# Performance work log

Hardware: AMD Instinct MI355X
Metric: run time of the kernel (lower is better)

Reference implementation:

```python
import jax, jax.numpy as jnp
import numpy as np

HIDDEN = 1024
N_EXPERTS = 8
CAP_FACTOR = 1.1
LN_EPS = 1e-5


def setup_inputs() -> dict:
    key = jax.random.key(0)
    ks = jax.random.split(key, 8)
    d, E, dff = HIDDEN, N_EXPERTS, 4 * HIDDEN
    x = jax.random.normal(ks[0], (4, 2048, d), dtype=jnp.float32)
    gate_w = jax.random.normal(ks[1], (d, E), dtype=jnp.float32) / np.sqrt(d)
    ln_g = jnp.ones((E, d), dtype=jnp.float32)
    ln_b = jnp.zeros((E, d), dtype=jnp.float32)
    w1 = jax.random.normal(ks[2], (E, d, dff), dtype=jnp.float32) / np.sqrt(d)
    b1 = jnp.zeros((E, dff), dtype=jnp.float32)
    w2 = jax.random.normal(ks[3], (E, dff, d), dtype=jnp.float32) / np.sqrt(dff)
    b2 = jnp.zeros((E, d), dtype=jnp.float32)
    return {"x": x, "gate_w": gate_w, "ln_g": ln_g, "ln_b": ln_b,
            "w1": w1, "b1": b1, "w2": w2, "b2": b2}


def reference(x, gate_w, ln_g, ln_b, w1, b1, w2, b2):
    B, S, d = x.shape
    E = gate_w.shape[1]
    N = B * S
    cap = int(N / E * CAP_FACTOR)  # expert capacity

    xt = x.reshape(N, d)
    # Router: top-1 expert per token (max-subtract before softmax is a no-op)
    logits = xt @ gate_w                               # [N, E]
    probs = jax.nn.softmax(logits, axis=-1)
    eidx = jnp.argmax(probs, axis=-1)                  # [N] int

    onehot = jax.nn.one_hot(eidx, E, dtype=jnp.int32)  # [N, E]
    counts = onehot.sum(axis=0).astype(jnp.float32)    # pre-drop counts [E]

    # Deterministic capacity: keep first `cap` tokens per expert, drop rest.
    # (torch code drops randomly via multinomial; structure is identical.)
    pos = jnp.cumsum(onehot, axis=0) - 1               # [N, E]
    pos_tok = jnp.take_along_axis(pos, eidx[:, None], axis=1)[:, 0]  # [N]
    keep = (pos_tok < cap).astype(x.dtype)             # [N]
    pos_c = jnp.minimum(pos_tok, cap - 1)              # clamp; dropped tokens write zeros

    # Dispatch into per-expert buffers [E, cap, d]
    buf = jnp.zeros((E, cap, d), dtype=x.dtype).at[eidx, pos_c].add(xt * keep[:, None])

    # Per-expert FFN: LayerNorm -> Linear -> GELU -> Linear
    mu = buf.mean(axis=-1, keepdims=True)
    var = jnp.mean((buf - mu) ** 2, axis=-1, keepdims=True)
    nb = (buf - mu) * jax.lax.rsqrt(var + LN_EPS)
    nb = nb * ln_g[:, None, :] + ln_b[:, None, :]
    h = jax.nn.gelu(jnp.einsum('ecd,edf->ecf', nb, w1) + b1[:, None, :], approximate=False)
    y = jnp.einsum('ecf,efd->ecd', h, w2) + b2[:, None, :]  # [E, cap, d]

    # Combine: dropped tokens get zeros (matches torch output init)
    out_tok = y[eidx, pos_c] * keep[:, None]           # [N, d]
    output = out_tok.reshape(B, S, d)

    # Load-balancing loss: 1 - cosine(counts, uniform) * 0.01
    tokens_per_expert = N / E
    uniform = jnp.full((E,), tokens_per_expert, dtype=jnp.float32)
    cos = jnp.dot(counts, uniform) / (jnp.linalg.norm(counts) * jnp.linalg.norm(uniform) + 1e-8)
    loss = 1.0 - cos * 0.01
    return output, loss
```

## Files before the change

kernel.cpp:

```cpp
#include <hip/hip_runtime.h>
#include <cstdint>
#include <cstddef>

#define NTOK 8192
#define D    1024
#define DFF  4096
#define NEXP 8
#define CAP  1126
#define MROWS 1280

typedef float f32x4 __attribute__((ext_vector_type(4)));
typedef __bf16 bf16x8 __attribute__((ext_vector_type(8)));

__device__ inline unsigned short f2bf(float f) {
    unsigned u = __float_as_uint(f);
    u += 0x7fffu + ((u >> 16) & 1u);
    return (unsigned short)(u >> 16);
}

__device__ inline float gelu(float x) {
    float z  = 0.70710678118654752f * x;
    float az = fabsf(z);
    float t  = 1.0f / fmaf(0.3275911f, az, 1.0f);
    float p  = t * fmaf(t, fmaf(t, fmaf(t, fmaf(t, 1.061405429f, -1.453152027f),
                                        1.421413741f), -0.284496736f), 0.254829592f);
    float ee = __expf(-az * az);
    float er = fmaf(-p, ee, 1.0f);
    er = __builtin_copysignf(er, z);
    return 0.5f * x * (1.0f + er);
}

__device__ inline void gload16(const void* g, void* l) {
    __builtin_amdgcn_global_load_lds(
        (const __attribute__((address_space(1))) unsigned int*)g,
        (__attribute__((address_space(3))) unsigned int*)l,
        16, 0, 0);
}

__device__ void transpose_tile_dev(const float* __restrict__ W, unsigned short* __restrict__ WT,
                                   int K, int N, int tb, char* smem)
{
    int tiles_k = K >> 7, tiles_n = N >> 7;
    int per_e = tiles_k * tiles_n;
    int e = tb / per_e, rem = tb % per_e;
    int kb = rem % tiles_k, nb = rem / tiles_k;
    const float* We = W + (size_t)e * K * N + (size_t)(kb * 128) * N + nb * 128;
    unsigned short* Oe = WT + (size_t)e * K * N + (size_t)(nb * 128) * K + kb * 128;
    float* lds = (float*)smem;
    int t = threadIdx.x;
    #pragma unroll
    for (int p = 0; p < 2; ++p) {
        __syncthreads();
        #pragma unroll
        for (int j = 0; j < 8; ++j) {
            int idx = j * 256 + t;
            int r = idx >> 5, c4 = idx & 31;
            const float4 v = *(const float4*)(We + (size_t)(p * 64 + r) * N + c4 * 4);
            *(float4*)(lds + r * 128 + c4 * 4) = v;
        }
        __syncthreads();
        int c = t >> 1, half = t & 1;
        const float* col = lds + (half * 32) * 128 + c;
        unsigned short* orow = Oe + (size_t)c * K + p * 64 + half * 32;
        #pragma unroll
        for (int q = 0; q < 4; ++q) {
            uint4 o;
            o.x = f2bf(col[(q*8+0)*128]) | ((unsigned)f2bf(col[(q*8+1)*128]) << 16);
            o.y = f2bf(col[(q*8+2)*128]) | ((unsigned)f2bf(col[(q*8+3)*128]) << 16);
            o.z = f2bf(col[(q*8+4)*128]) | ((unsigned)f2bf(col[(q*8+5)*128]) << 16);
            o.w = f2bf(col[(q*8+6)*128]) | ((unsigned)f2bf(col[(q*8+7)*128]) << 16);
            *(uint4*)(orow + q * 8) = o;
        }
    }
}

__global__ __launch_bounds__(256) void transpose_kernel(
    const float* __restrict__ W, unsigned short* __restrict__ WT, int K, int N)
{
    __shared__ __align__(16) char smem[32768];
    transpose_tile_dev(W, WT, K, N, blockIdx.x, smem);
}

__global__ __launch_bounds__(256) void router_kernel(
    const float* __restrict__ x, const float* __restrict__ gw, int* __restrict__ eidx)
{
    int tok  = blockIdx.x * 4 + (threadIdx.x >> 6);
    int lane = threadIdx.x & 63;
    const float* xr = x + (size_t)tok * D;
    float a[8] = {0.f,0.f,0.f,0.f,0.f,0.f,0.f,0.f};
    #pragma unroll
    for (int it = 0; it < D / 64; ++it) {
        int d = lane + it * 64;
        float xv = xr[d];
        const float4 g0 = *(const float4*)(gw + (size_t)d * 8);
        const float4 g1 = *(const float4*)(gw + (size_t)d * 8 + 4);
        a[0] += xv * g0.x; a[1] += xv * g0.y; a[2] += xv * g0.z; a[3] += xv * g0.w;
        a[4] += xv * g1.x; a[5] += xv * g1.y; a[6] += xv * g1.z; a[7] += xv * g1.w;
    }
    #pragma unroll
    for (int off = 32; off > 0; off >>= 1)
        #pragma unroll
        for (int e = 0; e < 8; ++e) a[e] += __shfl_xor(a[e], off, 64);
    if (lane == 0) {
        int bi = 0; float bv = a[0];
        #pragma unroll
        for (int e = 1; e < 8; ++e) if (a[e] > bv) { bv = a[e]; bi = e; }
        eidx[tok] = bi;
    }
}

__global__ __launch_bounds__(1024) void scan_kernel(
    const int* __restrict__ eidx, int* __restrict__ slot_map,
    int* __restrict__ kept_cnt, float* __restrict__ loss_out,
    int* __restrict__ droplist, int* __restrict__ dropcnt)
{
    __shared__ int sc[8][1024];
    __shared__ int dcnt;
    int t = threadIdx.x;
    if (t == 0) dcnt = 0;
    int le[8];
    int c[8] = {0,0,0,0,0,0,0,0};
    #pragma unroll
    for (int i = 0; i < 8; ++i) { le[i] = eidx[t * 8 + i]; c[le[i]]++; }
    int v[8];
    #pragma unroll
    for (int e = 0; e < 8; ++e) { v[e] = c[e]; sc[e][t] = v[e]; }
    __syncthreads();
    for (int s = 1; s < 1024; s <<= 1) {
        int add[8] = {0,0,0,0,0,0,0,0};
        if (t >= s) {
            #pragma unroll
            for (int e = 0; e < 8; ++e) add[e] = sc[e][t - s];
        }
        __syncthreads();
        #pragma unroll
        for (int e = 0; e < 8; ++e) { v[e] += add[e]; sc[e][t] = v[e]; }
        __syncthreads();
    }
    int base[8];
    #pragma unroll
    for (int e = 0; e < 8; ++e) base[e] = v[e] - c[e];
    #pragma unroll
    for (int i = 0; i < 8; ++i) {
        int e = le[i]; int pos = base[e]++;
        if (pos < CAP) slot_map[e * CAP + pos] = t * 8 + i;
        else { int s = atomicAdd(&dcnt, 1); droplist[s] = t * 8 + i; }
    }
    __syncthreads();
    if (t == 0) *dropcnt = dcnt;
    if (t == 1023) {
        float dotv = 0.f, ss = 0.f;
        #pragma unroll
        for (int e = 0; e < 8; ++e) {
            float cf = (float)v[e];
            kept_cnt[e] = v[e] < CAP ? v[e] : CAP;
            dotv += cf * 1024.0f;
            ss   += cf * cf;
        }
        float denom = sqrtf(ss) * (1024.0f * sqrtf(8.0f)) + 1e-8f;
        loss_out[0] = 1.0f - 0.01f * (dotv / denom);
    }
}

__global__ __launch_bounds__(256) void zero_dropped(
    const int* __restrict__ droplist, const int* __restrict__ dropcnt,
    float4* __restrict__ out)
{
    int n = (*dropcnt) * 256;
    for (int idx = blockIdx.x * 256 + threadIdx.x; idx < n; idx += gridDim.x * 256)
        out[(size_t)droplist[idx >> 8] * 256 + (idx & 255)] = make_float4(0.f,0.f,0.f,0.f);
}

__global__ __launch_bounds__(256) void dispatch_ln(
    const float* __restrict__ x, const float* __restrict__ lng, const float* __restrict__ lnb,
    const int* __restrict__ slot_map, const int* __restrict__ kept_cnt,
    unsigned short* __restrict__ xbuf)
{
    int p = blockIdx.x, e = blockIdx.y, tid = threadIdx.x;
    ushort4* dst = (ushort4*)(xbuf + ((size_t)e * MROWS + p) * D) + tid;
    if (p >= kept_cnt[e]) { *dst = make_ushort4(0, 0, 0, 0); return; }
    int tok = slot_map[e * CAP + p];
    const float4 xv = *((const float4*)(x + (size_t)tok * D) + tid);
    float s  = xv.x + xv.y + xv.z + xv.w;
    float ss = xv.x * xv.x + xv.y * xv.y + xv.z * xv.z + xv.w * xv.w;
    #pragma unroll
    for (int off = 32; off > 0; off >>= 1) {
        s  += __shfl_xor(s,  off, 64);
        ss += __shfl_xor(ss, off, 64);
    }
    __shared__ float red[8];
    int lane = tid & 63, wv = tid >> 6;
    if (lane == 0) { red[wv] = s; red[4 + wv] = ss; }
    __syncthreads();
    s  = red[0] + red[1] + red[2] + red[3];
    ss = red[4] + red[5] + red[6] + red[7];
    float mu = s * (1.0f / D);
    float rs = rsqrtf(ss * (1.0f / D) - mu * mu + 1e-5f);
    const float4 gv = *((const float4*)(lng + (size_t)e * D) + tid);
    const float4 bv = *((const float4*)(lnb + (size_t)e * D) + tid);
    ushort4 o;
    o.x = f2bf((xv.x - mu) * rs * gv.x + bv.x);
    o.y = f2bf((xv.y - mu) * rs * gv.y + bv.y);
    o.z = f2bf((xv.z - mu) * rs * gv.z + bv.z);
    o.w = f2bf((xv.w - mu) * rs * gv.w + bv.w);
    *dst = o;
}

template<int K, int N, int MODE>
__global__ __launch_bounds__(512, 2) void gemm_kernel(
    const unsigned short* __restrict__ A,
    const unsigned short* __restrict__ BT,
    const float* __restrict__ bias,
    unsigned short* __restrict__ Hout,
    float* __restrict__ Yout,
    const int* __restrict__ slot_map,
    const int* __restrict__ kept_cnt)
{
    constexpr int MB = MROWS / 256;
    constexpr int NB = N / 256;
    constexpr int GB = NEXP * MB * NB;
    constexpr int T  = K / 64;
    __shared__ __align__(16) char smem[131072];

    const int obid = blockIdx.x;
    const int q8 = GB >> 3, r8 = GB & 7;
    const int xcd = obid & 7, ii = obid >> 3;
    const int swz = (xcd < r8 ? xcd * (q8 + 1) : r8 * (q8 + 1) + (xcd - r8) * q8) + ii;
    const int mb = swz % MB;
    const int t2 = swz / MB;
    const int nb = t2 % NB;
    const int e  = t2 / NB;

    const int tid  = threadIdx.x;
    const int lane = tid & 63;
    const int l15  = lane & 15, lg = lane >> 4;
    const int wave = tid >> 6;
    const int wr = wave >> 2, wc = wave & 3;
    const unsigned short* Ae = A + ((size_t)e * MROWS + (size_t)mb * 256) * K;
    const unsigned short* Be = BT + ((size_t)e * N + (size_t)nb * 256) * K;
    f32x4 acc[8][4] = {};

    auto stageAB = [&](int buf, int kk) {
        char* sA = smem + buf * 65536;
        char* sB = sA + 32768;
        #pragma unroll
        for (int q = 0; q < 4; ++q) {
            int cid = q * 512 + tid;
            int row = cid >> 3, pp = cid & 7;
            int cc  = pp ^ ((row >> 1) & 7);
            gload16(Ae + (size_t)row * K + kk * 64 + cc * 8, sA + cid * 16);
            gload16(Be + (size_t)row * K + kk * 64 + cc * 8, sB + cid * 16);
        }
    };
    auto quad_load = [&](const char* sA, const char* sB, int mh, int nh,
                         bf16x8 (&af)[2][4], bf16x8 (&bfv)[2][2]) {
        #pragma unroll
        for (int i = 0; i < 4; ++i) {
            int ra = wr * 128 + mh * 64 + i * 16 + l15;
            #pragma unroll
            for (int ks = 0; ks < 2; ++ks)
                af[ks][i] = *(const bf16x8*)(sA + ra * 128 +
                             (((ks * 4 + lg) ^ ((ra >> 1) & 7)) << 4));
        }
        #pragma unroll
        for (int jn = 0; jn < 2; ++jn) {
            int rb = wc * 64 + nh * 32 + jn * 16 + l15;
            #pragma unroll
            for (int ks = 0; ks < 2; ++ks)
                bfv[ks][jn] = *(const bf16x8*)(sB + rb * 128 +
                             (((ks * 4 + lg) ^ ((rb >> 1) & 7)) << 4));
        }
    };
    auto quad_mfma = [&](int mh, int nh, bf16x8 (&af)[2][4], bf16x8 (&bfv)[2][2]) {
        __builtin_amdgcn_s_setprio(1);
        #pragma unroll
        for (int ks = 0; ks < 2; ++ks)
            #pragma unroll
            for (int i = 0; i < 4; ++i)
                #pragma unroll
                for (int jn = 0; jn < 2; ++jn)
                    acc[mh * 4 + i][nh * 2 + jn] = __builtin_amdgcn_mfma_f32_16x16x32_bf16(
                        bfv[ks][jn], af[ks][i], acc[mh * 4 + i][nh * 2 + jn], 0, 0, 0);
        __builtin_amdgcn_s_setprio(0);
    };

    stageAB(0, 0);
    stageAB(1, 1);
    asm volatile("s_waitcnt vmcnt(8)" ::: "memory");
    __builtin_amdgcn_s_barrier();

    for (int t = 0; t < T; ++t) {
        const char* sA = smem + (t & 1) * 65536;
        const char* sB = sA + 32768;
        bf16x8 af[2][4]; bf16x8 bfv[2][2];
        quad_load(sA, sB, 0, 0, af, bfv);  quad_mfma(0, 0, af, bfv);
        __builtin_amdgcn_sched_barrier(0);
        quad_load(sA, sB, 0, 1, af, bfv);  quad_mfma(0, 1, af, bfv);
        __builtin_amdgcn_sched_barrier(0);
        quad_load(sA, sB, 1, 0, af, bfv);  quad_mfma(1, 0, af, bfv);
        __builtin_amdgcn_sched_barrier(0);
        quad_load(sA, sB, 1, 1, af, bfv);
        asm volatile("s_waitcnt lgkmcnt(0)" ::: "memory");
        __builtin_amdgcn_sched_barrier(0);
        __builtin_amdgcn_s_barrier();
        if (t + 2 < T) stageAB(t & 1, t + 2);
        __builtin_amdgcn_sched_barrier(0);
        quad_mfma(1, 1, af, bfv);
        if (t < T - 1) {
            if (t + 2 < T) asm volatile("s_waitcnt vmcnt(8)" ::: "memory");
            else           asm volatile("s_waitcnt vmcnt(0)" ::: "memory");
            __builtin_amdgcn_s_barrier();
        }
    }

    const int kept = (MODE == 1) ? kept_cnt[e] : 0;
    #pragma unroll
    for (int mi = 0; mi < 8; ++mi) {
        const int row = mb * 256 + wr * 128 + mi * 16 + l15;
        int tok = 0; bool live = true;
        if (MODE == 1) {
            live = row < kept;
            tok = live ? slot_map[e * CAP + row] : 0;
        }
        #pragma unroll
        for (int ni = 0; ni < 4; ++ni) {
            const int colb = nb * 256 + wc * 64 + ni * 16 + 4 * lg;
            const float4 bv = *(const float4*)(bias + (size_t)e * N + colb);
            if (MODE == 0) {
                ushort4 o;
                o.x = f2bf(gelu(acc[mi][ni][0] + bv.x));
                o.y = f2bf(gelu(acc[mi][ni][1] + bv.y));
                o.z = f2bf(gelu(acc[mi][ni][2] + bv.z));
                o.w = f2bf(gelu(acc[mi][ni][3] + bv.w));
                *(ushort4*)(Hout + ((size_t)e * MROWS + row) * N + colb) = o;
            } else if (live) {
                float4 o = make_float4(acc[mi][ni][0] + bv.x, acc[mi][ni][1] + bv.y,
                                       acc[mi][ni][2] + bv.z, acc[mi][ni][3] + bv.w);
                *(float4*)(Yout + (size_t)tok * D + colb) = o;
            }
        }
    }
}

extern "C" void kernel_launch(void* const* d_in, const int* in_sizes, int n_in,
                              void* d_out, int out_size, void* d_ws, size_t ws_size,
                              hipStream_t stream)
{
    const float* x   = (const float*)d_in[0];
    const float* gw  = (const float*)d_in[1];
    const float* lng = (const float*)d_in[2];
    const float* lnb = (const float*)d_in[3];
    const float* w1  = (const float*)d_in[4];
    const float* b1  = (const float*)d_in[5];
    const float* w2  = (const float*)d_in[6];
    const float* b2  = (const float*)d_in[7];
    float* out = (float*)d_out;
    char* ws = (char*)d_ws;

    unsigned short* wT   = (unsigned short*)ws;
    unsigned short* xbuf = (unsigned short*)(ws + 67108864);
    unsigned short* hbuf = (unsigned short*)(ws + 88080384);
    int* eidx     = (int*)(ws + 171966464);
    int* slot_map = eidx + NTOK;
    int* kept     = slot_map + NEXP * CAP;
    int* dropcnt  = kept + NEXP;
    int* droplist = dropcnt + 8;

    constexpr int GB1 = NEXP * (MROWS / 256) * (DFF / 256);
    constexpr int GB2 = NEXP * (MROWS / 256) * (D / 256);
    constexpr int TB1 = NEXP * (D / 128) * (DFF / 128);
    constexpr int TB2 = NEXP * (DFF / 128) * (D / 128);

    router_kernel<<<NTOK / 4, 256, 0, stream>>>(x, gw, eidx);
    scan_kernel<<<1, 1024, 0, stream>>>(eidx, slot_map, kept,
                                        out + (size_t)NTOK * D, droplist, dropcnt);
    zero_dropped<<<64, 256, 0, stream>>>(droplist, dropcnt, (float4*)out);
    dispatch_ln<<<dim3(MROWS, NEXP), 256, 0, stream>>>(x, lng, lnb, slot_map, kept, xbuf);

    transpose_kernel<<<TB1, 256, 0, stream>>>(w1, wT, D, DFF);
    gemm_kernel<D, DFF, 0><<<GB1, 512, 0, stream>>>(
        xbuf, wT, b1, hbuf, nullptr, slot_map, kept);

    transpose_kernel<<<TB2, 256, 0, stream>>>(w2, wT, DFF, D);
    gemm_kernel<DFF, D, 1><<<GB2, 512, 0, stream>>>(
        hbuf, wT, b2, nullptr, out, slot_map, kept);
}
```

Baseline: 380.4 us.

## Switch expert GEMM to 32x32x16 MFMA tiles with two-phase LDS loads

Replaces the 16x16x32 bf16 MFMA with the 32x32x16 variant, so each wave computes its 128x64 tile as 4x2 blocks of 32x32 with 16-float accumulators. The four quarter-steps per K tile become two halves that each load all A/B fragments, then issue 16 MFMAs. Larger MFMA tiles cut LDS fragment reads and instruction count per FLOP. The cost is less overlap between LDS loads and MFMAs, and a changed epilogue mapping of accumulator lanes to output rows and columns.

```diff
diff --git a/kernel.cpp b/kernel.cpp
--- a/kernel.cpp
+++ b/kernel.cpp
@@ -9,7 +9,8 @@
 #define CAP  1126
 #define MROWS 1280
 
-typedef float f32x4 __attribute__((ext_vector_type(4)));
+typedef float f32x4  __attribute__((ext_vector_type(4)));
+typedef float f32x16 __attribute__((ext_vector_type(16)));
 typedef __bf16 bf16x8 __attribute__((ext_vector_type(8)));
 
 __device__ inline unsigned short f2bf(float f) {
@@ -233,12 +234,12 @@
 
     const int tid  = threadIdx.x;
     const int lane = tid & 63;
-    const int l15  = lane & 15, lg = lane >> 4;
+    const int l31  = lane & 31, hi = lane >> 5;
     const int wave = tid >> 6;
     const int wr = wave >> 2, wc = wave & 3;
     const unsigned short* Ae = A + ((size_t)e * MROWS + (size_t)mb * 256) * K;
     const unsigned short* Be = BT + ((size_t)e * N + (size_t)nb * 256) * K;
-    f32x4 acc[8][4] = {};
+    f32x16 acc[4][2] = {};
 
     auto stageAB = [&](int buf, int kk) {
         char* sA = smem + buf * 65536;
@@ -252,36 +253,15 @@
             gload16(Be + (size_t)row * K + kk * 64 + cc * 8, sB + cid * 16);
         }
     };
-    auto quad_load = [&](const char* sA, const char* sB, int mh, int nh,
-                         bf16x8 (&af)[2][4], bf16x8 (&bfv)[2][2]) {
-        #pragma unroll
-        for (int i = 0; i < 4; ++i) {
-            int ra = wr * 128 + mh * 64 + i * 16 + l15;
-            #pragma unroll
-            for (int ks = 0; ks < 2; ++ks)
-                af[ks][i] = *(const bf16x8*)(sA + ra * 128 +
-                             (((ks * 4 + lg) ^ ((ra >> 1) & 7)) << 4));
-        }
-        #pragma unroll
-        for (int jn = 0; jn < 2; ++jn) {
-            int rb = wc * 64 + nh * 32 + jn * 16 + l15;
-            #pragma unroll
-            for (int ks = 0; ks < 2; ++ks)
-                bfv[ks][jn] = *(const bf16x8*)(sB + rb * 128 +
-                             (((ks * 4 + lg) ^ ((rb >> 1) & 7)) << 4));
-        }
+    auto ldA = [&](const char* sA, int mblk, int ks) -> bf16x8 {
+        int row = wr * 128 + mblk * 32 + l31;
+        int c0  = 2 * ks + hi;
+        return *(const bf16x8*)(sA + row * 128 + ((c0 ^ ((row >> 1) & 7)) << 4));
     };
-    auto quad_mfma = [&](int mh, int nh, bf16x8 (&af)[2][4], bf16x8 (&bfv)[2][2]) {
-        __builtin_amdgcn_s_setprio(1);
-        #pragma unroll
-        for (int ks = 0; ks < 2; ++ks)
-            #pragma unroll
-            for (int i = 0; i < 4; ++i)
-                #pragma unroll
-                for (int jn = 0; jn < 2; ++jn)
-                    acc[mh * 4 + i][nh * 2 + jn] = __builtin_amdgcn_mfma_f32_16x16x32_bf16(
-                        bfv[ks][jn], af[ks][i], acc[mh * 4 + i][nh * 2 + jn], 0, 0, 0);
-        __builtin_amdgcn_s_setprio(0);
+    auto ldB = [&](const char* sB, int nblk, int ks) -> bf16x8 {
+        int row = wc * 64 + nblk * 32 + l31;
+        int c0  = 2 * ks + hi;
+        return *(const bf16x8*)(sB + row * 128 + ((c0 ^ ((row >> 1) & 7)) << 4));
     };
 
     stageAB(0, 0);
@@ -292,20 +272,43 @@
     for (int t = 0; t < T; ++t) {
         const char* sA = smem + (t & 1) * 65536;
         const char* sB = sA + 32768;
-        bf16x8 af[2][4]; bf16x8 bfv[2][2];
-        quad_load(sA, sB, 0, 0, af, bfv);  quad_mfma(0, 0, af, bfv);
+        bf16x8 af[4][2], bfv[2][2];
+        #pragma unroll
+        for (int m = 0; m < 4; ++m) { af[m][0] = ldA(sA, m, 0); af[m][1] = ldA(sA, m, 1); }
+        #pragma unroll
+        for (int n = 0; n < 2; ++n) { bfv[n][0] = ldB(sB, n, 0); bfv[n][1] = ldB(sB, n, 1); }
+        asm volatile("s_waitcnt lgkmcnt(0)" ::: "memory");
         __builtin_amdgcn_sched_barrier(0);
-        quad_load(sA, sB, 0, 1, af, bfv);  quad_mfma(0, 1, af, bfv);
+        __builtin_amdgcn_s_setprio(1);
+        #pragma unroll
+        for (int ks = 0; ks < 2; ++ks)
+            #pragma unroll
+            for (int m = 0; m < 4; ++m)
+                #pragma unroll
+                for (int n = 0; n < 2; ++n)
+                    acc[m][n] = __builtin_amdgcn_mfma_f32_32x32x16_bf16(
+                        bfv[n][ks], af[m][ks], acc[m][n], 0, 0, 0);
+        __builtin_amdgcn_s_setprio(0);
         __builtin_amdgcn_sched_barrier(0);
-        quad_load(sA, sB, 1, 0, af, bfv);  quad_mfma(1, 0, af, bfv);
-        __builtin_amdgcn_sched_barrier(0);
-        quad_load(sA, sB, 1, 1, af, bfv);
+        #pragma unroll
+        for (int m = 0; m < 4; ++m) { af[m][0] = ldA(sA, m, 2); af[m][1] = ldA(sA, m, 3); }
+        #pragma unroll
+        for (int n = 0; n < 2; ++n) { bfv[n][0] = ldB(sB, n, 2); bfv[n][1] = ldB(sB, n, 3); }
         asm volatile("s_waitcnt lgkmcnt(0)" ::: "memory");
         __builtin_amdgcn_sched_barrier(0);
         __builtin_amdgcn_s_barrier();
         if (t + 2 < T) stageAB(t & 1, t + 2);
         __builtin_amdgcn_sched_barrier(0);
-        quad_mfma(1, 1, af, bfv);
+        __builtin_amdgcn_s_setprio(1);
+        #pragma unroll
+        for (int ks = 0; ks < 2; ++ks)
+            #pragma unroll
+            for (int m = 0; m < 4; ++m)
+                #pragma unroll
+                for (int n = 0; n < 2; ++n)
+                    acc[m][n] = __builtin_amdgcn_mfma_f32_32x32x16_bf16(
+                        bfv[n][ks], af[m][ks], acc[m][n], 0, 0, 0);
+        __builtin_amdgcn_s_setprio(0);
         if (t < T - 1) {
             if (t + 2 < T) asm volatile("s_waitcnt vmcnt(8)" ::: "memory");
             else           asm volatile("s_waitcnt vmcnt(0)" ::: "memory");
@@ -315,28 +318,31 @@
 
     const int kept = (MODE == 1) ? kept_cnt[e] : 0;
     #pragma unroll
-    for (int mi = 0; mi < 8; ++mi) {
-        const int row = mb * 256 + wr * 128 + mi * 16 + l15;
+    for (int m = 0; m < 4; ++m) {
+        const int row = mb * 256 + wr * 128 + m * 32 + l31;
         int tok = 0; bool live = true;
         if (MODE == 1) {
             live = row < kept;
             tok = live ? slot_map[e * CAP + row] : 0;
         }
         #pragma unroll
-        for (int ni = 0; ni < 4; ++ni) {
-            const int colb = nb * 256 + wc * 64 + ni * 16 + 4 * lg;
-            const float4 bv = *(const float4*)(bias + (size_t)e * N + colb);
-            if (MODE == 0) {
-                ushort4 o;
-                o.x = f2bf(gelu(acc[mi][ni][0] + bv.x));
-                o.y = f2bf(gelu(acc[mi][ni][1] + bv.y));
-                o.z = f2bf(gelu(acc[mi][ni][2] + bv.z));
-                o.w = f2bf(gelu(acc[mi][ni][3] + bv.w));
-                *(ushort4*)(Hout + ((size_t)e * MROWS + row) * N + colb) = o;
-            } else if (live) {
-                float4 o = make_float4(acc[mi][ni][0] + bv.x, acc[mi][ni][1] + bv.y,
-                                       acc[mi][ni][2] + bv.z, acc[mi][ni][3] + bv.w);
-                *(float4*)(Yout + (size_t)tok * D + colb) = o;
+        for (int n = 0; n < 2; ++n) {
+            #pragma unroll
+            for (int q = 0; q < 4; ++q) {
+                const int colb = nb * 256 + wc * 64 + n * 32 + q * 8 + hi * 4;
+                const float4 bv = *(const float4*)(bias + (size_t)e * N + colb);
+                float v0 = acc[m][n][4*q+0] + bv.x;
+                float v1 = acc[m][n][4*q+1] + bv.y;
+                float v2 = acc[m][n][4*q+2] + bv.z;
+                float v3 = acc[m][n][4*q+3] + bv.w;
+                if (MODE == 0) {
+                    ushort4 o;
+                    o.x = f2bf(gelu(v0)); o.y = f2bf(gelu(v1));
+                    o.z = f2bf(gelu(v2)); o.w = f2bf(gelu(v3));
+                    *(ushort4*)(Hout + ((size_t)e * MROWS + row) * N + colb) = o;
+                } else if (live) {
+                    *(float4*)(Yout + (size_t)tok * D + colb) = make_float4(v0, v1, v2, v3);
+                }
             }
         }
     }
```

Measured after the change: 374.8 us. Within noise of the previous version (-1.5%).
